# Performance work log

Measured on AMD Instinct MI355X. Metric: run time of the kernel, lower is better.

## Reference

```python
import jax, jax.numpy as jnp
import numpy as np

EPS = 1e-5


def _conv1x1(x, w, b):
    # x: (B,C,H,W), w: (O,C), b: (O,)
    return jnp.einsum('bchw,oc->bohw', x, w) + b[None, :, None, None]


def setup_inputs() -> dict:
    key = jax.random.key(0)
    ks = jax.random.split(key, 12)
    C, Ci = 512, 256
    B, H, W = 4, 64, 64
    s_in = 1.0 / np.sqrt(C)
    s_ci = 1.0 / np.sqrt(Ci)
    return {
        'x': jax.random.normal(ks[0], (B, C, H, W), dtype=jnp.float32),
        'g_w': jax.random.normal(ks[1], (Ci, C), dtype=jnp.float32) * s_in,
        'g_b': jax.random.normal(ks[2], (Ci,), dtype=jnp.float32) * 0.01,
        'theta_w': jax.random.normal(ks[3], (Ci, C), dtype=jnp.float32) * s_in,
        'theta_b': jax.random.normal(ks[4], (Ci,), dtype=jnp.float32) * 0.01,
        'phi_w': jax.random.normal(ks[5], (Ci, C), dtype=jnp.float32) * s_in,
        'phi_b': jax.random.normal(ks[6], (Ci,), dtype=jnp.float32) * 0.01,
        'W_w': jax.random.normal(ks[7], (C, Ci), dtype=jnp.float32) * s_ci,
        'W_b': jax.random.normal(ks[8], (C,), dtype=jnp.float32) * 0.01,
        'bn_gamma': jax.random.normal(ks[9], (C,), dtype=jnp.float32) * 0.1,
        'bn_beta': jax.random.normal(ks[10], (C,), dtype=jnp.float32) * 0.01,
    }


def reference(x, g_w, g_b, theta_w, theta_b, phi_w, phi_b, W_w, W_b, bn_gamma, bn_beta):
    B, C, H, W = x.shape
    Ci = g_w.shape[0]
    HW = H * W
    # 1x1-conv projections -> token form
    g = _conv1x1(x, g_w, g_b).reshape(B, Ci, HW).transpose(0, 2, 1)        # (B,HW,Ci)
    theta = _conv1x1(x, theta_w, theta_b).reshape(B, Ci, HW).transpose(0, 2, 1)  # (B,HW,Ci)
    phi = _conv1x1(x, phi_w, phi_b).reshape(B, Ci, HW)                      # (B,Ci,HW)
    # dense HWxHW attention, scaled by sqrt(inter_channels)
    pairwise = jnp.einsum('bnc,bcm->bnm', theta, phi) / jnp.sqrt(jnp.float32(Ci))
    attn = jax.nn.softmax(pairwise, axis=-1)
    y = jnp.einsum('bnm,bmc->bnc', attn, g)                                 # (B,HW,Ci)
    y = y.transpose(0, 2, 1).reshape(B, Ci, H, W)
    # output 1x1 conv + BatchNorm2d (training-mode batch statistics)
    z = _conv1x1(y, W_w, W_b)
    mean = jnp.mean(z, axis=(0, 2, 3), keepdims=True)
    var = jnp.var(z, axis=(0, 2, 3), keepdims=True)
    z = bn_gamma[None, :, None, None] * (z - mean) * jax.lax.rsqrt(var + EPS) + bn_beta[None, :, None, None]
    return z + x
```

## Files before the change

kernel.cpp:

```cpp
#include <hip/hip_runtime.h>

typedef unsigned short u16;
typedef __attribute__((ext_vector_type(4))) u16 u16x4;
typedef __attribute__((ext_vector_type(8))) u16 u16x8;
typedef __attribute__((ext_vector_type(8))) short s16x8;
typedef __attribute__((ext_vector_type(4))) float f32x4;

#define B_  4
#define C_  512
#define CI_ 256
#define HW_ 4096

static __device__ __forceinline__ u16 f2bf(float f) {
  unsigned u = __float_as_uint(f);
  return (u16)((u + 0x7FFFu + ((u >> 16) & 1u)) >> 16);
}
static __device__ __forceinline__ float bf2f(u16 h) {
  return __uint_as_float(((unsigned)h) << 16);
}

static __device__ __forceinline__ f32x4 mfma16(s16x8 a, s16x8 b, f32x4 c) {
  return __builtin_amdgcn_mfma_f32_16x16x32_bf16(a, b, c, 0, 0, 0);
}

typedef __attribute__((address_space(3))) unsigned int as3_u32;
typedef const __attribute__((address_space(1))) unsigned int as1_u32;
static __device__ __forceinline__ void gload16(const u16* g, u16* l) {
  __builtin_amdgcn_global_load_lds((as1_u32*)g, (as3_u32*)l, 16, 0, 0);
}

__global__ __launch_bounds__(256) void k0_wcvt(
    const float* __restrict__ wg, const float* __restrict__ wt,
    const float* __restrict__ wp, const float* __restrict__ Ww,
    u16* __restrict__ wB, u16* __restrict__ WwB)
{
  int idx = (blockIdx.x * 256 + threadIdx.x) * 8;
  const float* src;
  u16* dst;
  if (idx < 393216) {
    int r = idx >> 17;
    src = (r == 0 ? wg : r == 1 ? wt : wp) + (idx & 131071);
    dst = wB + idx;
  } else {
    src = Ww + (idx - 393216);
    dst = WwB + (idx - 393216);
  }
  float4 v0 = *reinterpret_cast<const float4*>(src);
  float4 v1 = *reinterpret_cast<const float4*>(src + 4);
  u16x8 h;
  h[0] = f2bf(v0.x); h[1] = f2bf(v0.y); h[2] = f2bf(v0.z); h[3] = f2bf(v0.w);
  h[4] = f2bf(v1.x); h[5] = f2bf(v1.y); h[6] = f2bf(v1.z); h[7] = f2bf(v1.w);
  *reinterpret_cast<u16x8*>(dst) = h;
}

__global__ __launch_bounds__(256) void k0_xt(
    const float* __restrict__ x, u16* __restrict__ xT, int b0)
{
  __shared__ u16 lds[64][72];
  const int tid = threadIdx.x;
  const int n0 = blockIdx.x * 64, c0 = blockIdx.y * 64;
  const int bl = blockIdx.z;
  const int b = b0 + bl;
  const int nc = (tid & 15) * 4;
#pragma unroll
  for (int i = 0; i < 4; ++i) {
    int cr = (tid >> 4) + i * 16;
    float4 v = *reinterpret_cast<const float4*>(
        &x[((size_t)(b * C_ + c0 + cr)) * HW_ + n0 + nc]);
    u16x4 h; h[0] = f2bf(v.x); h[1] = f2bf(v.y); h[2] = f2bf(v.z); h[3] = f2bf(v.w);
    *reinterpret_cast<u16x4*>(&lds[cr][nc]) = h;
  }
  __syncthreads();
  const int n = tid & 63, cg = tid >> 6;
  u16x8 o0, o1;
#pragma unroll
  for (int j = 0; j < 8; ++j) { o0[j] = lds[cg * 16 + j][n]; o1[j] = lds[cg * 16 + 8 + j][n]; }
  size_t dstb = ((size_t)bl * HW_ + n0 + n) * C_ + c0 + cg * 16;
  *reinterpret_cast<u16x8*>(&xT[dstb])     = o0;
  *reinterpret_cast<u16x8*>(&xT[dstb + 8]) = o1;
}

__global__ __launch_bounds__(256) void k1_proj(
    const u16* __restrict__ wB, const u16* __restrict__ xT,
    const float* __restrict__ bg, const float* __restrict__ bt, const float* __restrict__ bp,
    u16* __restrict__ g_s, u16* __restrict__ thetaT, u16* __restrict__ phiT, int half)
{
  extern __shared__ u16 sm1[];
  const int tid = threadIdx.x;
  const int lane = tid & 63, wid = tid >> 6;
  const int wm = wid >> 1, wn = wid & 1;
  const int l15 = lane & 15, g4 = lane >> 4;

  const int bid = blockIdx.x;
  const int r12 = bid % 12;
  const int nt = bid / 12;
  const int mt = r12 >> 1;
  const int bl = r12 & 1;
  const int b = half * 2 + bl;
  const int m0 = mt * 128, n0g = nt * 128;
  const int p = mt >> 1;

  const u16* xb = xT + (size_t)bl * HW_ * C_;

  const int srow = tid >> 2, sch = tid & 3;
  const u16* a_src = wB + (size_t)(m0 + srow) * C_ + sch * 8;
  const u16* b_src = xb + (size_t)(n0g + srow) * C_ + sch * 8;

  f32x4 acc[4][4] = {};

  auto stage1 = [&](int buf, int ks) {
    u16* d = sm1 + buf * 8192;
#pragma unroll
    for (int i = 0; i < 2; ++i) {
      gload16(a_src + (size_t)(i * 64) * C_ + ks * 32, d + (tid + i * 256) * 8);
      gload16(b_src + (size_t)(i * 64) * C_ + ks * 32, d + 4096 + (tid + i * 256) * 8);
    }
  };
  auto compute1 = [&](int buf) {
    const u16* A = sm1 + buf * 8192;
    const u16* Bt = A + 4096;
    s16x8 afr[4], bfr[4];
#pragma unroll
    for (int mf = 0; mf < 4; ++mf)
      afr[mf] = *reinterpret_cast<const s16x8*>(&A[(wm * 64 + mf * 16 + l15) * 32 + g4 * 8]);
#pragma unroll
    for (int nf = 0; nf < 4; ++nf)
      bfr[nf] = *reinterpret_cast<const s16x8*>(&Bt[(wn * 64 + nf * 16 + l15) * 32 + g4 * 8]);
#pragma unroll
    for (int mf = 0; mf < 4; ++mf)
#pragma unroll
      for (int nf = 0; nf < 4; ++nf)
        acc[mf][nf] = mfma16(afr[mf], bfr[nf], acc[mf][nf]);
  };

  stage1(0, 0); stage1(1, 1);
  int cur = 0;
#pragma unroll 1
  for (int ks = 0; ks < 15; ++ks) {
    asm volatile("s_waitcnt vmcnt(4)" ::: "memory");
    __builtin_amdgcn_s_barrier();
    compute1(cur);
    if (ks < 14) { int nb = cur + 2; if (nb >= 3) nb -= 3; stage1(nb, ks + 2); }
    cur = (cur == 2) ? 0 : cur + 1;
  }
  asm volatile("s_waitcnt vmcnt(0)" ::: "memory");
  __builtin_amdgcn_s_barrier();
  compute1(cur);
  __syncthreads();

  const float* bias = (p == 0) ? bg : (p == 1) ? bt : bp;
  const int cib = (mt & 1) * 128;
#pragma unroll
  for (int mf = 0; mf < 4; ++mf)
#pragma unroll
    for (int r = 0; r < 4; ++r) {
      float bv = bias[cib + wm * 64 + mf * 16 + g4 * 4 + r];
#pragma unroll
      for (int nf = 0; nf < 4; ++nf) acc[mf][nf][r] += bv;
    }

  if (p == 0) {
    u16* lds_t = sm1;
#pragma unroll
    for (int mf = 0; mf < 4; ++mf)
#pragma unroll
      for (int nf = 0; nf < 4; ++nf)
#pragma unroll
        for (int r = 0; r < 4; ++r)
          lds_t[(wm * 64 + mf * 16 + g4 * 4 + r) * 136 + wn * 64 + nf * 16 + l15] =
              f2bf(acc[mf][nf][r]);
    __syncthreads();
    const int m = tid >> 1, hh = tid & 1;
    size_t dst = ((size_t)b * CI_ + cib + m) * HW_ + n0g + hh * 64;
#pragma unroll
    for (int j = 0; j < 8; ++j)
      *reinterpret_cast<u16x8*>(&g_s[dst + j * 8]) =
          *reinterpret_cast<const u16x8*>(&lds_t[m * 136 + hh * 64 + j * 8]);
  } else {
    u16* outp = (p == 1) ? thetaT : phiT;
#pragma unroll
    for (int mf = 0; mf < 4; ++mf)
#pragma unroll
      for (int nf = 0; nf < 4; ++nf) {
        u16x4 h;
#pragma unroll
        for (int r = 0; r < 4; ++r) h[r] = f2bf(acc[mf][nf][r]);
        int n = n0g + wn * 64 + nf * 16 + l15;
        *reinterpret_cast<u16x4*>(
            &outp[((size_t)b * HW_ + n) * CI_ + cib + wm * 64 + mf * 16 + g4 * 4]) = h;
      }
  }
}

#define OFF_PHI0 0
#define OFF_PHI1 16384
#define OFF_G0   32768
#define OFF_G1   49152
#define OFF_PB0  65536
#define OFF_PB1  70144
#define OFF_LP   74752

__global__ __launch_bounds__(512) void k3_fused(
    const u16* __restrict__ thetaT, const u16* __restrict__ phiT,
    const u16* __restrict__ g_s, u16* __restrict__ y)
{
  extern __shared__ u16 smem[];
  float* Lp = (float*)(smem + OFF_LP);
  float* iL = Lp + 256;

  const int tid = threadIdx.x;
  const int lane = tid & 63, w = tid >> 6;
  const int l15 = lane & 15, g4 = lane >> 4;

  const int bid = blockIdx.x;
  const int xcd = bid & 7, slot = bid >> 3;
  const int b  = xcd >> 1;
  const int n0 = ((xcd & 1) * 32 + slot) * 64;

  const int ms = w >> 1, nh = w & 1;
  const int cq = w >> 1, nh2 = w & 1;

  const u16* thb = thetaT + (size_t)b * HW_ * CI_;
  const u16* phb = phiT   + (size_t)b * HW_ * CI_;
  const u16* gsb = g_s    + (size_t)b * CI_ * HW_;

  s16x8 thfr[2][8];
#pragma unroll
  for (int nf = 0; nf < 2; ++nf)
#pragma unroll
    for (int cs = 0; cs < 8; ++cs)
      thfr[nf][cs] = *reinterpret_cast<const s16x8*>(
          &thb[(size_t)(n0 + nh * 32 + nf * 16 + l15) * CI_ + cs * 32 + g4 * 8]);

  const int prow = tid >> 5, pj = tid & 31;
  const int grow = tid >> 3, gj = tid & 7;
  const u16* ph_src = phb + (size_t)prow * CI_ + ((pj ^ (prow & 7)) * 8);
  const u16* g_src  = gsb + (size_t)grow * HW_ + ((gj ^ (grow & 7)) * 8);
  const int ph_do = prow * 256 + pj * 8;
  const int g_do  = grow * 64  + gj * 8;

  auto stage_phi = [&](int off, int mt) {
#pragma unroll
    for (int i = 0; i < 4; ++i)
      gload16(ph_src + (size_t)(mt + i * 16) * CI_, smem + off + ph_do + i * 4096);
  };
  auto stage_g = [&](int off, int mt) {
#pragma unroll
    for (int i = 0; i < 4; ++i)
      gload16(g_src + mt + (size_t)i * 64 * HW_, smem + off + g_do + i * 4096);
  };

  f32x4 oacc[2][4] = {};
  float psum[2] = {0.f, 0.f};

  auto qk_phase = [&](const u16* phN, u16* pbN) {
    f32x4 acc[2] = {};
    __builtin_amdgcn_s_setprio(1);
#pragma unroll
    for (int cs = 0; cs < 8; ++cs) {
      s16x8 a = *reinterpret_cast<const s16x8*>(
          &phN[(ms * 16 + l15) * 256 + (((cs * 4 + g4) ^ (l15 & 7)) * 8)]);
      acc[0] = mfma16(a, thfr[0][cs], acc[0]);
      acc[1] = mfma16(a, thfr[1][cs], acc[1]);
    }
    __builtin_amdgcn_s_setprio(0);
#pragma unroll
    for (int nf = 0; nf < 2; ++nf) {
      u16x4 pk;
#pragma unroll
      for (int r = 0; r < 4; ++r) {
        float e = __expf(acc[nf][r] * 0.0625f);
        psum[nf] += e;
        pk[r] = f2bf(e);
      }
      *reinterpret_cast<u16x4*>(&pbN[(nh * 32 + nf * 16 + l15) * 72 + ms * 16 + g4 * 4]) = pk;
    }
  };
  auto pv_phase = [&](const u16* pbC, const u16* gC) {
    __builtin_amdgcn_s_setprio(1);
#pragma unroll
    for (int mk = 0; mk < 2; ++mk) {
      s16x8 pa[2];
#pragma unroll
      for (int nf = 0; nf < 2; ++nf)
        pa[nf] = *reinterpret_cast<const s16x8*>(
            &pbC[(nh2 * 32 + nf * 16 + l15) * 72 + mk * 32 + g4 * 8]);
#pragma unroll
      for (int cf = 0; cf < 4; ++cf) {
        int crow = cq * 64 + cf * 16 + l15;
        s16x8 bb = *reinterpret_cast<const s16x8*>(
            &gC[crow * 64 + (((mk * 4 + g4) ^ (crow & 7)) * 8)]);
        oacc[0][cf] = mfma16(pa[0], bb, oacc[0][cf]);
        oacc[1][cf] = mfma16(pa[1], bb, oacc[1][cf]);
      }
    }
    __builtin_amdgcn_s_setprio(0);
  };

  stage_phi(OFF_PHI0, 0); stage_g(OFF_G0, 0);
  stage_phi(OFF_PHI1, 64); stage_g(OFF_G1, 64);
  asm volatile("s_waitcnt vmcnt(0)" ::: "memory");
  __builtin_amdgcn_s_barrier();
  qk_phase(smem + OFF_PHI0, smem + OFF_PB0);
  asm volatile("s_waitcnt lgkmcnt(0)" ::: "memory");
  __builtin_amdgcn_s_barrier();

#pragma unroll 1
  for (int it = 0; it < 62; ++it) {
    const int cur = it & 1;
    stage_phi(cur ? OFF_PHI1 : OFF_PHI0, (it + 2) * 64);
    asm volatile("s_waitcnt vmcnt(8)" ::: "memory");
    __builtin_amdgcn_s_barrier();
    qk_phase(smem + (cur ? OFF_PHI0 : OFF_PHI1),
             smem + (cur ? OFF_PB0 : OFF_PB1));
    pv_phase(smem + (cur ? OFF_PB1 : OFF_PB0),
             smem + (cur ? OFF_G1 : OFF_G0));
    asm volatile("s_waitcnt lgkmcnt(0)" ::: "memory");
    __builtin_amdgcn_s_barrier();
    stage_g(cur ? OFF_G1 : OFF_G0, (it + 2) * 64);
  }
  asm volatile("s_waitcnt vmcnt(4)" ::: "memory");
  __builtin_amdgcn_s_barrier();
  qk_phase(smem + OFF_PHI1, smem + OFF_PB1);
  pv_phase(smem + OFF_PB0, smem + OFF_G0);
  asm volatile("s_waitcnt lgkmcnt(0)" ::: "memory");
  __builtin_amdgcn_s_barrier();
  asm volatile("s_waitcnt vmcnt(0)" ::: "memory");
  __builtin_amdgcn_s_barrier();
  pv_phase(smem + OFF_PB1, smem + OFF_G1);

#pragma unroll
  for (int nf = 0; nf < 2; ++nf) {
    psum[nf] += __shfl_xor(psum[nf], 16);
    psum[nf] += __shfl_xor(psum[nf], 32);
  }
  if (lane < 16) {
    Lp[ms * 64 + nh * 32 + lane]      = psum[0];
    Lp[ms * 64 + nh * 32 + 16 + lane] = psum[1];
  }
  __syncthreads();
  if (tid < 64) iL[tid] = 1.0f / (Lp[tid] + Lp[64 + tid] + Lp[128 + tid] + Lp[192 + tid]);
  __syncthreads();

  u16* yb = y + ((size_t)b * HW_ + n0) * CI_;
#pragma unroll
  for (int nf = 0; nf < 2; ++nf)
#pragma unroll
    for (int r = 0; r < 4; ++r) {
      int nl = nh2 * 32 + nf * 16 + g4 * 4 + r;
      float il = iL[nl];
#pragma unroll
      for (int cf = 0; cf < 4; ++cf)
        yb[(size_t)nl * CI_ + cq * 64 + cf * 16 + l15] = f2bf(oacc[nf][cf][r] * il);
    }
}

__global__ __launch_bounds__(256) void k4_wconv(
    const u16* __restrict__ WwB, const u16* __restrict__ y, const float* __restrict__ Wb,
    u16* __restrict__ z, float* __restrict__ zsum, float* __restrict__ zsq)
{
  extern __shared__ u16 sm4[];
  __shared__ float lds_ps[2][128][2];
  const int tid = threadIdx.x;
  const int lane = tid & 63, wid = tid >> 6;
  const int wm = wid >> 1, wn = wid & 1;
  const int l15 = lane & 15, g4 = lane >> 4;

  const int bid = blockIdx.x;
  const int xcd = bid & 7, slot = bid >> 3;
  const int b = xcd >> 1, half = xcd & 1;
  const int mt = slot & 3;
  const int nt = half * 16 + (slot >> 2);
  const int o0 = mt * 128, n0g = nt * 128;

  const int srow = tid >> 2, sch = tid & 3;
  const u16* a_src = WwB + (size_t)(o0 + srow) * CI_ + sch * 8;
  const u16* b_src = y + ((size_t)(b * HW_ + n0g + srow)) * CI_ + sch * 8;

  f32x4 acc[4][4] = {};

  auto stage4 = [&](int buf, int ks) {
    u16* d = sm4 + buf * 8192;
#pragma unroll
    for (int i = 0; i < 2; ++i) {
      gload16(a_src + (size_t)(i * 64) * CI_ + ks * 32, d + (tid + i * 256) * 8);
      gload16(b_src + (size_t)(i * 64) * CI_ + ks * 32, d + 4096 + (tid + i * 256) * 8);
    }
  };
  auto compute4 = [&](int buf) {
    const u16* A = sm4 + buf * 8192;
    const u16* Bt = A + 4096;
    s16x8 afr[4], bfr[4];
#pragma unroll
    for (int mf = 0; mf < 4; ++mf)
      afr[mf] = *reinterpret_cast<const s16x8*>(&A[(wm * 64 + mf * 16 + l15) * 32 + g4 * 8]);
#pragma unroll
    for (int nf = 0; nf < 4; ++nf)
      bfr[nf] = *reinterpret_cast<const s16x8*>(&Bt[(wn * 64 + nf * 16 + l15) * 32 + g4 * 8]);
#pragma unroll
    for (int mf = 0; mf < 4; ++mf)
#pragma unroll
      for (int nf = 0; nf < 4; ++nf)
        acc[mf][nf] = mfma16(afr[mf], bfr[nf], acc[mf][nf]);
  };

  stage4(0, 0); stage4(1, 1);
  int cur = 0;
#pragma unroll 1
  for (int ks = 0; ks < 7; ++ks) {
    asm volatile("s_waitcnt vmcnt(4)" ::: "memory");
    __builtin_amdgcn_s_barrier();
    compute4(cur);
    if (ks < 6) { int nb = cur + 2; if (nb >= 3) nb -= 3; stage4(nb, ks + 2); }
    cur = (cur == 2) ? 0 : cur + 1;
  }
  asm volatile("s_waitcnt vmcnt(0)" ::: "memory");
  __builtin_amdgcn_s_barrier();
  compute4(cur);
  __syncthreads();

  u16* lds_t = sm4;
#pragma unroll
  for (int mf = 0; mf < 4; ++mf)
#pragma unroll
    for (int r = 0; r < 4; ++r) {
      const int ol = wm * 64 + mf * 16 + g4 * 4 + r;
      float wb = Wb[o0 + ol];
      float s = 0.f, q = 0.f;
#pragma unroll
      for (int nf = 0; nf < 4; ++nf) {
        float zv = acc[mf][nf][r] + wb;
        s += zv; q += zv * zv;
        lds_t[ol * 136 + wn * 64 + nf * 16 + l15] = f2bf(zv);
      }
      s += __shfl_xor(s, 1); s += __shfl_xor(s, 2); s += __shfl_xor(s, 4); s += __shfl_xor(s, 8);
      q += __shfl_xor(q, 1); q += __shfl_xor(q, 2); q += __shfl_xor(q, 4); q += __shfl_xor(q, 8);
      if (l15 == 0) { lds_ps[wn][ol][0] = s; lds_ps[wn][ol][1] = q; }
    }
  __syncthreads();
  {
    const int m = tid >> 1, hh = tid & 1;
    size_t dst = ((size_t)(b * C_ + o0 + m)) * HW_ + n0g + hh * 64;
#pragma unroll
    for (int j = 0; j < 8; ++j)
      *reinterpret_cast<u16x8*>(&z[dst + j * 8]) =
          *reinterpret_cast<const u16x8*>(&lds_t[m * 136 + hh * 64 + j * 8]);
  }
  if (tid < 128) {
    int col = b * 32 + nt;
    zsum[(size_t)(o0 + tid) * 128 + col] = lds_ps[0][tid][0] + lds_ps[1][tid][0];
    zsq [(size_t)(o0 + tid) * 128 + col] = lds_ps[0][tid][1] + lds_ps[1][tid][1];
  }
}

__global__ void k5_bnstat(const float* __restrict__ zsum, const float* __restrict__ zsq,
                          const float* __restrict__ gamma, const float* __restrict__ beta,
                          float* __restrict__ bns, float* __restrict__ bnb)
{
  int ch = blockIdx.x * 256 + threadIdx.x;
  if (ch >= C_) return;
  float s = 0.f, q = 0.f;
  for (int i = 0; i < 128; ++i) { s += zsum[(size_t)ch * 128 + i]; q += zsq[(size_t)ch * 128 + i]; }
  const float inv_n = 1.0f / (B_ * HW_);
  float mean = s * inv_n;
  float var  = q * inv_n - mean * mean;
  float sc = gamma[ch] * rsqrtf(var + 1e-5f);
  bns[ch] = sc;
  bnb[ch] = beta[ch] - mean * sc;
}

__global__ __launch_bounds__(256) void k6_final(
    const u16* __restrict__ z, const float* __restrict__ x,
    const float* __restrict__ bns, const float* __restrict__ bnb,
    float* __restrict__ out)
{
  size_t i = ((size_t)blockIdx.x * 256 + threadIdx.x) * 8;
  int ch = (int)((i >> 12) & 511);
  float sc = bns[ch], sh = bnb[ch];
  u16x8 zv = *reinterpret_cast<const u16x8*>(&z[i]);
  float4 x0 = *reinterpret_cast<const float4*>(&x[i]);
  float4 x1 = *reinterpret_cast<const float4*>(&x[i + 4]);
  float4 o0, o1;
  o0.x = bf2f(zv[0]) * sc + sh + x0.x;
  o0.y = bf2f(zv[1]) * sc + sh + x0.y;
  o0.z = bf2f(zv[2]) * sc + sh + x0.z;
  o0.w = bf2f(zv[3]) * sc + sh + x0.w;
  o1.x = bf2f(zv[4]) * sc + sh + x1.x;
  o1.y = bf2f(zv[5]) * sc + sh + x1.y;
  o1.z = bf2f(zv[6]) * sc + sh + x1.z;
  o1.w = bf2f(zv[7]) * sc + sh + x1.w;
  *reinterpret_cast<float4*>(&out[i])     = o0;
  *reinterpret_cast<float4*>(&out[i + 4]) = o1;
}

extern "C" void kernel_launch(void* const* d_in, const int* in_sizes, int n_in,
                              void* d_out, int out_size, void* d_ws, size_t ws_size,
                              hipStream_t stream)
{
  (void)in_sizes; (void)n_in; (void)out_size; (void)ws_size;
  const float* x    = (const float*)d_in[0];
  const float* g_w  = (const float*)d_in[1];
  const float* g_b  = (const float*)d_in[2];
  const float* t_w  = (const float*)d_in[3];
  const float* t_b  = (const float*)d_in[4];
  const float* p_w  = (const float*)d_in[5];
  const float* p_b  = (const float*)d_in[6];
  const float* W_w  = (const float*)d_in[7];
  const float* W_b  = (const float*)d_in[8];
  const float* bng  = (const float*)d_in[9];
  const float* bnb_ = (const float*)d_in[10];

  char* ws = (char*)d_ws;
  const size_t M8 = (size_t)8 << 20;
  u16*   xT     = (u16*)(ws + 0);
  u16*   y      = (u16*)(ws + 0);
  u16*   thetaT = (u16*)(ws + M8);
  u16*   phiT   = (u16*)(ws + 2 * M8);
  u16*   g_s    = (u16*)(ws + 3 * M8);
  u16*   zbf    = (u16*)(ws + M8);
  float* zsum   = (float*)(ws + 3 * M8);
  float* zsq    = (float*)(ws + 3 * M8 + 262144);
  float* bnsV   = (float*)(ws + 3 * M8 + 524288);
  float* bnbV   = (float*)(ws + 3 * M8 + 526336);
  u16*   wB     = (u16*)(ws + 4 * M8);
  u16*   WwB    = (u16*)(ws + 4 * M8 + 786432);
  float* out    = (float*)d_out;

  const int k1_lds = 49152;
  const int k3_lds = 150784;
  const int k4_lds = 49152;
  hipFuncSetAttribute(reinterpret_cast<const void*>(k1_proj),
                      hipFuncAttributeMaxDynamicSharedMemorySize, k1_lds);
  hipFuncSetAttribute(reinterpret_cast<const void*>(k3_fused),
                      hipFuncAttributeMaxDynamicSharedMemorySize, k3_lds);
  hipFuncSetAttribute(reinterpret_cast<const void*>(k4_wconv),
                      hipFuncAttributeMaxDynamicSharedMemorySize, k4_lds);

  hipLaunchKernelGGL(k0_wcvt, dim3(256), dim3(256), 0, stream,
                     g_w, t_w, p_w, W_w, wB, WwB);
  for (int half = 0; half < 2; ++half) {
    hipLaunchKernelGGL(k0_xt, dim3(64, 8, 2), dim3(256), 0, stream, x, xT, half * 2);
    hipLaunchKernelGGL(k1_proj, dim3(384), dim3(256), k1_lds, stream,
                       wB, xT, g_b, t_b, p_b, g_s, thetaT, phiT, half);
  }
  hipLaunchKernelGGL(k3_fused, dim3(256), dim3(512), k3_lds, stream,
                     thetaT, phiT, g_s, y);
  hipLaunchKernelGGL(k4_wconv, dim3(512), dim3(256), k4_lds, stream,
                     WwB, y, W_b, zbf, zsum, zsq);
  hipLaunchKernelGGL(k5_bnstat, dim3(2), dim3(256), 0, stream,
                     zsum, zsq, bng, bnb_, bnsV, bnbV);
  hipLaunchKernelGGL(k6_final, dim3(4096), dim3(256), 0, stream,
                     zbf, x, bnsV, bnbV, out);
}
```

Before: 198.0 us.

## Read phi directly from global and single-buffer g tiles in fused attention kernel

Removes the LDS staging and double buffering of phi tiles in the fused attention kernel. Phi fragments are now loaded straight from global memory into registers for the QK MFMAs, and g uses a single LDS buffer refilled after each PV step, with plain __syncthreads in place of hand-tuned waitcnts. LDS use drops sharply and launch bounds now request 4 blocks per CU. The cost is lost overlap between loads and compute, uncached strided global reads for phi, and register pressure from the tighter launch bounds, which risks spills given the large theta fragment array. With only 256 blocks, higher occupancy may also gain little.

```diff
diff --git a/kernel.cpp b/kernel.cpp
--- a/kernel.cpp
+++ b/kernel.cpp
@@ -192,15 +192,12 @@
   }
 }
 
-#define OFF_PHI0 0
-#define OFF_PHI1 16384
-#define OFF_G0   32768
-#define OFF_G1   49152
-#define OFF_PB0  65536
-#define OFF_PB1  70144
-#define OFF_LP   74752
-
-__global__ __launch_bounds__(512) void k3_fused(
+#define OFF_G    0
+#define OFF_PB0  16384
+#define OFF_PB1  20992
+#define OFF_LP   25600
+
+__global__ __launch_bounds__(512, 4) void k3_fused(
     const u16* __restrict__ thetaT, const u16* __restrict__ phiT,
     const u16* __restrict__ g_s, u16* __restrict__ y)
 {
@@ -232,38 +229,28 @@
       thfr[nf][cs] = *reinterpret_cast<const s16x8*>(
           &thb[(size_t)(n0 + nh * 32 + nf * 16 + l15) * CI_ + cs * 32 + g4 * 8]);
 
-  const int prow = tid >> 5, pj = tid & 31;
   const int grow = tid >> 3, gj = tid & 7;
-  const u16* ph_src = phb + (size_t)prow * CI_ + ((pj ^ (prow & 7)) * 8);
-  const u16* g_src  = gsb + (size_t)grow * HW_ + ((gj ^ (grow & 7)) * 8);
-  const int ph_do = prow * 256 + pj * 8;
-  const int g_do  = grow * 64  + gj * 8;
-
-  auto stage_phi = [&](int off, int mt) {
+  const u16* g_src = gsb + (size_t)grow * HW_ + ((gj ^ (grow & 7)) * 8);
+  const int g_do   = grow * 64 + gj * 8;
+
+  auto stage_g = [&](int mt) {
 #pragma unroll
     for (int i = 0; i < 4; ++i)
-      gload16(ph_src + (size_t)(mt + i * 16) * CI_, smem + off + ph_do + i * 4096);
-  };
-  auto stage_g = [&](int off, int mt) {
-#pragma unroll
-    for (int i = 0; i < 4; ++i)
-      gload16(g_src + mt + (size_t)i * 64 * HW_, smem + off + g_do + i * 4096);
+      gload16(g_src + mt + (size_t)i * 64 * HW_, smem + OFF_G + g_do + i * 4096);
   };
 
   f32x4 oacc[2][4] = {};
   float psum[2] = {0.f, 0.f};
 
-  auto qk_phase = [&](const u16* phN, u16* pbN) {
+  auto qk_it = [&](int t, u16* pbN) {
+    const u16* ph = phb + ((size_t)(t * 64 + ms * 16 + l15)) * CI_;
     f32x4 acc[2] = {};
-    __builtin_amdgcn_s_setprio(1);
 #pragma unroll
     for (int cs = 0; cs < 8; ++cs) {
-      s16x8 a = *reinterpret_cast<const s16x8*>(
-          &phN[(ms * 16 + l15) * 256 + (((cs * 4 + g4) ^ (l15 & 7)) * 8)]);
+      s16x8 a = *reinterpret_cast<const s16x8*>(&ph[cs * 32 + g4 * 8]);
       acc[0] = mfma16(a, thfr[0][cs], acc[0]);
       acc[1] = mfma16(a, thfr[1][cs], acc[1]);
     }
-    __builtin_amdgcn_s_setprio(0);
 #pragma unroll
     for (int nf = 0; nf < 2; ++nf) {
       u16x4 pk;
@@ -276,7 +263,8 @@
       *reinterpret_cast<u16x4*>(&pbN[(nh * 32 + nf * 16 + l15) * 72 + ms * 16 + g4 * 4]) = pk;
     }
   };
-  auto pv_phase = [&](const u16* pbC, const u16* gC) {
+  auto pv_phase = [&](const u16* pbC) {
+    const u16* gC = smem + OFF_G;
     __builtin_amdgcn_s_setprio(1);
 #pragma unroll
     for (int mk = 0; mk < 2; ++mk) {
@@ -297,37 +285,21 @@
     __builtin_amdgcn_s_setprio(0);
   };
 
-  stage_phi(OFF_PHI0, 0); stage_g(OFF_G0, 0);
-  stage_phi(OFF_PHI1, 64); stage_g(OFF_G1, 64);
-  asm volatile("s_waitcnt vmcnt(0)" ::: "memory");
-  __builtin_amdgcn_s_barrier();
-  qk_phase(smem + OFF_PHI0, smem + OFF_PB0);
-  asm volatile("s_waitcnt lgkmcnt(0)" ::: "memory");
-  __builtin_amdgcn_s_barrier();
+  stage_g(0);
+  qk_it(0, smem + OFF_PB0);
+  __syncthreads();
 
 #pragma unroll 1
-  for (int it = 0; it < 62; ++it) {
+  for (int it = 0; it < 63; ++it) {
     const int cur = it & 1;
-    stage_phi(cur ? OFF_PHI1 : OFF_PHI0, (it + 2) * 64);
-    asm volatile("s_waitcnt vmcnt(8)" ::: "memory");
-    __builtin_amdgcn_s_barrier();
-    qk_phase(smem + (cur ? OFF_PHI0 : OFF_PHI1),
-             smem + (cur ? OFF_PB0 : OFF_PB1));
-    pv_phase(smem + (cur ? OFF_PB1 : OFF_PB0),
-             smem + (cur ? OFF_G1 : OFF_G0));
-    asm volatile("s_waitcnt lgkmcnt(0)" ::: "memory");
-    __builtin_amdgcn_s_barrier();
-    stage_g(cur ? OFF_G1 : OFF_G0, (it + 2) * 64);
-  }
-  asm volatile("s_waitcnt vmcnt(4)" ::: "memory");
-  __builtin_amdgcn_s_barrier();
-  qk_phase(smem + OFF_PHI1, smem + OFF_PB1);
-  pv_phase(smem + OFF_PB0, smem + OFF_G0);
-  asm volatile("s_waitcnt lgkmcnt(0)" ::: "memory");
-  __builtin_amdgcn_s_barrier();
-  asm volatile("s_waitcnt vmcnt(0)" ::: "memory");
-  __builtin_amdgcn_s_barrier();
-  pv_phase(smem + OFF_PB1, smem + OFF_G1);
+    qk_it(it + 1, smem + (cur ? OFF_PB0 : OFF_PB1));
+    __syncthreads();
+    pv_phase(smem + (cur ? OFF_PB1 : OFF_PB0));
+    __syncthreads();
+    stage_g((it + 1) * 64);
+  }
+  __syncthreads();
+  pv_phase(smem + OFF_PB1);
 
 #pragma unroll
   for (int nf = 0; nf < 2; ++nf) {
@@ -527,7 +499,7 @@
   float* out    = (float*)d_out;
 
   const int k1_lds = 49152;
-  const int k3_lds = 150784;
+  const int k3_lds = 52480;
   const int k4_lds = 49152;
   hipFuncSetAttribute(reinterpret_cast<const void*>(k1_proj),
                       hipFuncAttributeMaxDynamicSharedMemorySize, k1_lds);
```

Result: slower. 342.4 us (+72.9%).
